# Performance work log

Hardware: AMD Instinct MI355X
Metric: run time of the kernel (lower is better)

The kernel has to match this reference:

```python
import jax, jax.numpy as jnp
import numpy as np

N = 50000          # nodes
E = 1_600_000      # edges (avg degree 32)
IN = 128           # in_channels
H1, C1 = 4, 8      # conv1: heads=4, out=8 -> concat 32
OUT = 64           # out_channels (conv2, heads=1)
NEG_SLOPE = 0.2    # PyG GATConv default LeakyReLU slope


def _gat_layer(x, edge_index, W, att_src, att_dst, bias, heads, out_ch):
    """PyG-style GATConv (concat=True, add_self_loops=True).
    x: [N, F_in], edge_index: [2, E], W: [F_in, heads*out_ch],
    att_src/att_dst: [heads, out_ch], bias: [heads*out_ch].
    """
    n = x.shape[0]
    loops = jnp.arange(n)
    src = jnp.concatenate([edge_index[0], loops])  # message source j
    dst = jnp.concatenate([edge_index[1], loops])  # aggregation target i

    h = (x @ W).reshape(n, heads, out_ch)                 # [N, H, C]
    a_src = jnp.sum(h * att_src, axis=-1)                 # [N, H]
    a_dst = jnp.sum(h * att_dst, axis=-1)                 # [N, H]

    logits = jax.nn.leaky_relu(a_src[src] + a_dst[dst], NEG_SLOPE)  # [E', H]
    # segment softmax over incoming edges of each destination node
    m = jax.ops.segment_max(logits, dst, num_segments=n)            # [N, H]
    e = jnp.exp(logits - m[dst])
    s = jax.ops.segment_sum(e, dst, num_segments=n)                 # [N, H]
    alpha = e / (s[dst] + 1e-16)                                    # [E', H]

    msg = h[src] * alpha[..., None]                                 # [E', H, C]
    out = jax.ops.segment_sum(msg, dst, num_segments=n)             # [N, H, C]
    return out.reshape(n, heads * out_ch) + bias


def setup_inputs() -> dict:
    key = jax.random.key(0)
    ks = jax.random.split(key, 10)
    g = 0.1
    x = jax.random.normal(ks[0], (N, IN), jnp.float32)
    edge_index = jax.random.randint(ks[1], (2, E), 0, N, dtype=jnp.int64)
    W1 = jax.random.normal(ks[2], (IN, H1 * C1), jnp.float32) * g
    att_src1 = jax.random.normal(ks[3], (H1, C1), jnp.float32) * g
    att_dst1 = jax.random.normal(ks[4], (H1, C1), jnp.float32) * g
    b1 = jnp.zeros((H1 * C1,), jnp.float32)
    W2 = jax.random.normal(ks[5], (H1 * C1, OUT), jnp.float32) * g
    att_src2 = jax.random.normal(ks[6], (1, OUT), jnp.float32) * g
    att_dst2 = jax.random.normal(ks[7], (1, OUT), jnp.float32) * g
    b2 = jnp.zeros((OUT,), jnp.float32)
    return {"x": x, "edge_index": edge_index,
            "W1": W1, "att_src1": att_src1, "att_dst1": att_dst1, "b1": b1,
            "W2": W2, "att_src2": att_src2, "att_dst2": att_dst2, "b2": b2}


def reference(x, edge_index, W1, att_src1, att_dst1, b1, W2, att_src2, att_dst2, b2):
    h = _gat_layer(x, edge_index, W1, att_src1, att_dst1, b1, H1, C1)   # [N, 32]
    h = jax.nn.relu(h)
    out = _gat_layer(h, edge_index, W2, att_src2, att_dst2, b2, 1, OUT)  # [N, 64]
    return out
```

## Files before the change

kernel.cpp:

```cpp
#include <hip/hip_runtime.h>
#include <hip/hip_bf16.h>

#define IN_CH 128
#define H1C1  32
#define NH1   4
#define OUTC  64
#define NEG   0.2f
#define RPAD  16
#define BSH   6
#define BSZ   64
#define NBMAX 1024
#define CHUNK 4096
#define CAP   3072
#define PCAP  4096
#define NPB   32

typedef __hip_bfloat16 bf16;
typedef unsigned int u32;
typedef unsigned short u16;

__device__ __forceinline__ u16 f2bf_bits(float f) {
  bf16 v = __float2bfloat16(f);
  return *(u16*)&v;
}
__device__ __forceinline__ float bflo(u32 g) { return __uint_as_float(g << 16); }
__device__ __forceinline__ float bfhi(u32 g) { return __uint_as_float(g & 0xFFFF0000u); }

__global__ __launch_bounds__(256) void k_bin_tr(
    const int* __restrict__ ei, int* __restrict__ bucket_fill,
    u32* __restrict__ data, int E, int n, int nb, int nA,
    const float* __restrict__ x, const float* __restrict__ W1,
    const float* __restrict__ as1, const float* __restrict__ ad1,
    u16* __restrict__ h1b, float* __restrict__ a_src, float* __restrict__ a_dst) {
  __shared__ __align__(16) char smem[28672];
  int t = threadIdx.x;
  if ((int)blockIdx.x < nA) {
    int* cnt   = (int*)smem;
    int* lbase = cnt + NBMAX;
    int* gbase = lbase + NBMAX;
    u32* staged = (u32*)(gbase + NBMAX);
    int lane = t & 63, wid = t >> 6;
    for (int b = t; b < nb; b += 256) cnt[b] = 0;
    __syncthreads();
    long base = (long)blockIdx.x * CHUNK;
    long totE = (long)E + n;
    u32 pk[CHUNK / 256];
    int bk[CHUNK / 256];
#pragma unroll
    for (int i = 0; i < CHUNK / 256; i++) {
      long e = base + i * 256 + t;
      if (e < totE) {
        int j, d;
        if (e < E) {
          j = ei[e]; d = ei[E + e];
          j = j < 0 ? 0 : (j >= n ? n - 1 : j);
          d = d < 0 ? 0 : (d >= n ? n - 1 : d);
        } else { j = d = (int)(e - E); }
        bk[i] = d >> BSH;
        pk[i] = ((u32)d << 16) | (u32)j;
        atomicAdd(&cnt[bk[i]], 1);
      } else bk[i] = -1;
    }
    __syncthreads();
    if (wid == 0) {
      int carry = 0;
      for (int b0 = 0; b0 < nb; b0 += 64) {
        int i = b0 + lane;
        int v = (i < nb) ? cnt[i] : 0;
        int orig = v;
        for (int off = 1; off < 64; off <<= 1) {
          int u = __shfl_up(v, off, 64);
          if (lane >= off) v += u;
        }
        if (i < nb) lbase[i] = carry + v - orig;
        carry += __shfl(v, 63, 64);
      }
    }
    __syncthreads();
    for (int b = t; b < nb; b += 256) {
      int c = cnt[b];
      gbase[b] = c ? atomicAdd(&bucket_fill[b], c) : 0;
      cnt[b] = 0;
    }
    __syncthreads();
#pragma unroll
    for (int i = 0; i < CHUNK / 256; i++) {
      if (bk[i] >= 0) {
        int loc = atomicAdd(&cnt[bk[i]], 1);
        staged[lbase[bk[i]] + loc] = pk[i];
      }
    }
    __syncthreads();
    long remL = totE - base;
    int rem = remL > CHUNK ? CHUNK : (int)remL;
    for (int idx = t; idx < rem; idx += 256) {
      u32 p = staged[idx];
      int b = (int)(p >> 16) >> BSH;
      int off2 = gbase[b] + (idx - lbase[b]);
      if (off2 < CAP) data[(size_t)b * CAP + off2] = p;
    }
  } else {
    float* xs = (float*)smem;
    int base = ((int)blockIdx.x - nA) * NPB;
    for (int i4 = t; i4 < NPB * 32; i4 += 256) {
      int nd = base + (i4 >> 5);
      float4 v = make_float4(0.f, 0.f, 0.f, 0.f);
      if (nd < n) v = ((const float4*)x)[(size_t)base * 32 + i4];
      ((float4*)xs)[i4] = v;
    }
    int mg = t & 7, ks = (t >> 3) & 7, ns = t >> 6;
    int m0 = mg * 4;
    float4 w[4][4];
#pragma unroll
    for (int kk = 0; kk < 4; kk++) {
      int q = (kk + ks) & 3;
      int k0 = ks * 16 + q * 4;
      float4 t0 = *(const float4*)(W1 + (k0 + 0) * H1C1 + m0);
      float4 t1 = *(const float4*)(W1 + (k0 + 1) * H1C1 + m0);
      float4 t2 = *(const float4*)(W1 + (k0 + 2) * H1C1 + m0);
      float4 t3 = *(const float4*)(W1 + (k0 + 3) * H1C1 + m0);
      w[kk][0] = make_float4(t0.x, t1.x, t2.x, t3.x);
      w[kk][1] = make_float4(t0.y, t1.y, t2.y, t3.y);
      w[kk][2] = make_float4(t0.z, t1.z, t2.z, t3.z);
      w[kk][3] = make_float4(t0.w, t1.w, t2.w, t3.w);
    }
    float4 asq = *(const float4*)(as1 + m0);
    float4 adq = *(const float4*)(ad1 + m0);
    __syncthreads();
#pragma unroll 2
    for (int r = 0; r < 8; r++) {
      int nl = r * 4 + ns;
      const float4* xrow = (const float4*)(xs + nl * IN_CH + ks * 16);
      float a0 = 0.f, a1 = 0.f, a2 = 0.f, a3 = 0.f;
#pragma unroll
      for (int kk = 0; kk < 4; kk++) {
        int q = (kk + ks) & 3;
        float4 xv = xrow[q];
        a0 += xv.x * w[kk][0].x + xv.y * w[kk][0].y + xv.z * w[kk][0].z + xv.w * w[kk][0].w;
        a1 += xv.x * w[kk][1].x + xv.y * w[kk][1].y + xv.z * w[kk][1].z + xv.w * w[kk][1].w;
        a2 += xv.x * w[kk][2].x + xv.y * w[kk][2].y + xv.z * w[kk][2].z + xv.w * w[kk][2].w;
        a3 += xv.x * w[kk][3].x + xv.y * w[kk][3].y + xv.z * w[kk][3].z + xv.w * w[kk][3].w;
      }
#pragma unroll
      for (int off = 8; off < 64; off <<= 1) {
        a0 += __shfl_xor(a0, off, 64);
        a1 += __shfl_xor(a1, off, 64);
        a2 += __shfl_xor(a2, off, 64);
        a3 += __shfl_xor(a3, off, 64);
      }
      int node = base + nl;
      if (ks == 0 && node < n) {
        float vs = a0 * asq.x + a1 * asq.y + a2 * asq.z + a3 * asq.w;
        float vd = a0 * adq.x + a1 * adq.y + a2 * adq.z + a3 * adq.w;
        vs += __shfl_xor(vs, 1, 64);
        vd += __shfl_xor(vd, 1, 64);
        u32 lo = (u32)f2bf_bits(a0) | ((u32)f2bf_bits(a1) << 16);
        u32 hi = (u32)f2bf_bits(a2) | ((u32)f2bf_bits(a3) << 16);
        *(uint2*)(h1b + (size_t)node * H1C1 + m0) = make_uint2(lo, hi);
        if ((mg & 1) == 0) {
          a_src[node * NH1 + (mg >> 1)] = vs;
          a_dst[node * NH1 + (mg >> 1)] = vd;
        }
      }
    }
    if ((int)blockIdx.x == nA) {
      if (t < H1C1) h1b[n * H1C1 + t] = 0;
      if (t < NH1)  a_src[n * NH1 + t] = -1e30f;
    }
  }
}

__global__ __launch_bounds__(256) void k_bucket_scatter(
    const u32* __restrict__ data, const int* __restrict__ bucket_fill,
    int2* __restrict__ rowse, int* __restrict__ col, int n) {
  __shared__ int cur[BSZ];
  __shared__ int rp[BSZ];
  __shared__ int pd[BSZ];
  int t = threadIdx.x;
  int b = blockIdx.x;
  if (t < BSZ) cur[t] = 0;
  __syncthreads();
  int s = b * CAP;
  int cnt = bucket_fill[b];
  if (cnt > CAP) cnt = CAP;
  for (int i = t; i < cnt; i += 256)
    atomicAdd(&cur[(data[s + i] >> 16) & (BSZ - 1)], 1);
  __syncthreads();
  if (t < 64) {
    int raw = cur[t];
    int v = (raw + RPAD - 1) & ~(RPAD - 1);
    int orig = v;
    for (int off = 1; off < 64; off <<= 1) {
      int u = __shfl_up(v, off, 64);
      if (t >= off) v += u;
    }
    int r = b * PCAP + v - orig;
    rp[t] = r;
    pd[t] = orig;
    cur[t] = r;
    int node = (b << BSH) + t;
    if (node < n) rowse[node] = make_int2(r, r + orig);
  }
  __syncthreads();
  for (int i = t; i < cnt; i += 256) {
    u32 p = data[s + i];
    int dl = (int)(p >> 16) & (BSZ - 1);
    int pos = atomicAdd(&cur[dl], 1);
    col[pos] = (int)(p & 0xFFFFu);
  }
  __syncthreads();
  if (t < 64) {
    int c = cur[t];
    int end = rp[t] + pd[t];
    for (int k = c; k < end; k++) col[k] = n;
  }
}

__global__ __launch_bounds__(256) void k_l1_agg(
    const int2* __restrict__ rowse, const int* __restrict__ col,
    const u16* __restrict__ h1b, const float* __restrict__ a_src,
    const float* __restrict__ a_dst, const float* __restrict__ b1,
    const float* __restrict__ W2, const float* __restrict__ as2,
    const float* __restrict__ ad2,
    u16* __restrict__ h2, float* __restrict__ a_src2, float* __restrict__ a_dst2,
    int n) {
  __shared__ float W2s[8 * 256];
  __shared__ float hsh[16][H1C1];
  __shared__ int   js[4][64];
  __shared__ float wsh[4][NH1][68];
  int t = threadIdx.x;
  int wid = t >> 6, lane = t & 63;
  {
    int c = t & 63;
#pragma unroll
    for (int g = 0; g < 2; g++) {
      int kg = (t >> 6) + 4 * g;
      float4 v;
      v.x = W2[(kg * 4 + 0) * OUTC + c];
      v.y = W2[(kg * 4 + 1) * OUTC + c];
      v.z = W2[(kg * 4 + 2) * OUTC + c];
      v.w = W2[(kg * 4 + 3) * OUTC + c];
      *(float4*)(W2s + kg * 256 + c * 4) = v;
    }
  }
  int o = lane >> 3, u = lane & 7;
  int hd = u >> 1;
  for (int s = 0; s < 4; s++) {
    int node = blockIdx.x * 16 + wid * 4 + s;
    if (node >= n) continue;
    int2 se = rowse[node];
    int rs = se.x, re = se.y;
    float4 ad = *(const float4*)(a_dst + node * NH1);
    float a0 = 0.f, a1 = 0.f, a2 = 0.f, a3 = 0.f, sw = 0.f;
    for (int tb = rs; tb < re; tb += 64) {
      int kmax = re - tb; if (kmax > 64) kmax = 64;
      if (lane < kmax) {
        int j = col[tb + lane];
        float4 as = *(const float4*)(a_src + j * NH1);
        float l0 = as.x + ad.x; l0 = l0 > 0.f ? l0 : NEG * l0;
        float l1 = as.y + ad.y; l1 = l1 > 0.f ? l1 : NEG * l1;
        float l2 = as.z + ad.z; l2 = l2 > 0.f ? l2 : NEG * l2;
        float l3 = as.w + ad.w; l3 = l3 > 0.f ? l3 : NEG * l3;
        js[wid][lane] = j;
        wsh[wid][0][lane] = __expf(l0);
        wsh[wid][1][lane] = __expf(l1);
        wsh[wid][2][lane] = __expf(l2);
        wsh[wid][3][lane] = __expf(l3);
      }
      int nbod = kmax >> 4;
      uint2 G0[4], G1[4];
      float W0[4], W1v[4];
#pragma unroll
      for (int b = 0; b < 4; b++) {
        if (b < nbod) {
          int k = b * 16;
          int j0 = js[wid][k + o];
          int j1 = js[wid][k + 8 + o];
          W0[b]  = wsh[wid][hd][k + o];
          W1v[b] = wsh[wid][hd][k + 8 + o];
          G0[b] = *(const uint2*)(h1b + j0 * H1C1 + 4 * u);
          G1[b] = *(const uint2*)(h1b + j1 * H1C1 + 4 * u);
        }
      }
#pragma unroll
      for (int b = 0; b < 4; b++) {
        if (b < nbod) {
          float w0 = W0[b], w1 = W1v[b];
          uint2 g0 = G0[b], g1 = G1[b];
          a0 += w0 * bflo(g0.x) + w1 * bflo(g1.x);
          a1 += w0 * bfhi(g0.x) + w1 * bfhi(g1.x);
          a2 += w0 * bflo(g0.y) + w1 * bflo(g1.y);
          a3 += w0 * bfhi(g0.y) + w1 * bfhi(g1.y);
          sw += w0 + w1;
        }
      }
    }
    for (int off = 8; off < 64; off <<= 1) {
      a0 += __shfl_xor(a0, off, 64);
      a1 += __shfl_xor(a1, off, 64);
      a2 += __shfl_xor(a2, off, 64);
      a3 += __shfl_xor(a3, off, 64);
      sw += __shfl_xor(sw, off, 64);
    }
    if (o == 0) {
      float inv = 1.f / (sw + 1e-16f);
      int c = 4 * u;
      hsh[wid * 4 + s][c]     = fmaxf(a0 * inv + b1[c], 0.f);
      hsh[wid * 4 + s][c + 1] = fmaxf(a1 * inv + b1[c + 1], 0.f);
      hsh[wid * 4 + s][c + 2] = fmaxf(a2 * inv + b1[c + 2], 0.f);
      hsh[wid * 4 + s][c + 3] = fmaxf(a3 * inv + b1[c + 3], 0.f);
    }
  }
  __syncthreads();
  float as2l = as2[lane], ad2l = ad2[lane];
  for (int r = 0; r < 4; r++) {
    int nl = wid * 4 + r;
    int node = blockIdx.x * 16 + nl;
    float acc = 0.f;
#pragma unroll
    for (int kg = 0; kg < 8; kg++) {
      float4 hv = *(const float4*)(&hsh[nl][kg * 4]);
      float4 wv = *(const float4*)(W2s + kg * 256 + lane * 4);
      acc += hv.x * wv.x + hv.y * wv.y + hv.z * wv.z + hv.w * wv.w;
    }
    float vs = acc * as2l;
    float vd = acc * ad2l;
    for (int off = 1; off < 64; off <<= 1) {
      vs += __shfl_xor(vs, off, 64);
      vd += __shfl_xor(vd, off, 64);
    }
    if (node < n) {
      h2[node * OUTC + lane] = f2bf_bits(acc);
      if (lane == 0) { a_src2[node] = vs; a_dst2[node] = vd; }
    }
  }
  if (blockIdx.x == 0) {
    if (t < OUTC) h2[n * OUTC + t] = 0;
    if (t == 0)   a_src2[n] = -1e30f;
  }
}

__global__ __launch_bounds__(256) void k_l2_agg(
    const int2* __restrict__ rowse, const int* __restrict__ col,
    const u16* __restrict__ h2, const float* __restrict__ a_src2,
    const float* __restrict__ a_dst2, const float* __restrict__ b2v,
    float* __restrict__ out, int n) {
  __shared__ int   js[4][64];
  __shared__ float wsh[4][64];
  int t = threadIdx.x;
  int wid = t >> 6, lane = t & 63;
  int o = lane >> 4, u = lane & 15;
  for (int s = 0; s < 4; s++) {
    int node = blockIdx.x * 16 + wid * 4 + s;
    if (node >= n) continue;
    int2 se = rowse[node];
    int rs = se.x, re = se.y;
    float ad = a_dst2[node];
    float a0 = 0.f, a1 = 0.f, a2 = 0.f, a3 = 0.f, sw = 0.f;
    for (int tb = rs; tb < re; tb += 64) {
      int kmax = re - tb; if (kmax > 64) kmax = 64;
      if (lane < kmax) {
        int j = col[tb + lane];
        float lg = a_src2[j] + ad;
        lg = lg > 0.f ? lg : NEG * lg;
        js[wid][lane] = j;
        wsh[wid][lane] = __expf(lg);
      }
      int nbod = kmax >> 4;
      for (int kb = 0; kb < nbod; kb += 2) {
        int np = (kb + 1 < nbod) ? 2 : 1;
        uint2 G[2][4];
        float W[2][4];
#pragma unroll
        for (int p = 0; p < 2; p++) {
          if (p < np) {
            int k = (kb + p) * 16;
#pragma unroll
            for (int q = 0; q < 4; q++) {
              int j = js[wid][k + 4 * q + o];
              W[p][q] = wsh[wid][k + 4 * q + o];
              G[p][q] = *(const uint2*)(h2 + j * OUTC + 4 * u);
            }
          }
        }
#pragma unroll
        for (int p = 0; p < 2; p++) {
          if (p < np) {
            a0 += W[p][0] * bflo(G[p][0].x) + W[p][1] * bflo(G[p][1].x);
            a0 += W[p][2] * bflo(G[p][2].x) + W[p][3] * bflo(G[p][3].x);
            a1 += W[p][0] * bfhi(G[p][0].x) + W[p][1] * bfhi(G[p][1].x);
            a1 += W[p][2] * bfhi(G[p][2].x) + W[p][3] * bfhi(G[p][3].x);
            a2 += W[p][0] * bflo(G[p][0].y) + W[p][1] * bflo(G[p][1].y);
            a2 += W[p][2] * bflo(G[p][2].y) + W[p][3] * bflo(G[p][3].y);
            a3 += W[p][0] * bfhi(G[p][0].y) + W[p][1] * bfhi(G[p][1].y);
            a3 += W[p][2] * bfhi(G[p][2].y) + W[p][3] * bfhi(G[p][3].y);
            sw += (W[p][0] + W[p][1]) + (W[p][2] + W[p][3]);
          }
        }
      }
    }
    for (int off = 16; off < 64; off <<= 1) {
      a0 += __shfl_xor(a0, off, 64);
      a1 += __shfl_xor(a1, off, 64);
      a2 += __shfl_xor(a2, off, 64);
      a3 += __shfl_xor(a3, off, 64);
      sw += __shfl_xor(sw, off, 64);
    }
    if (o == 0) {
      float inv = 1.f / (sw + 1e-16f);
      int c = 4 * u;
      float4 ov;
      ov.x = a0 * inv + b2v[c];
      ov.y = a1 * inv + b2v[c + 1];
      ov.z = a2 * inv + b2v[c + 2];
      ov.w = a3 * inv + b2v[c + 3];
      *(float4*)(out + node * OUTC + c) = ov;
    }
  }
}


extern "C" void kernel_launch(void* const* d_in, const int* in_sizes, int n_in,
                              void* d_out, int out_size, void* d_ws, size_t ws_size,
                              hipStream_t stream) {
  const float* x   = (const float*)d_in[0];
  const int*   ei  = (const int*)d_in[1];
  const float* W1  = (const float*)d_in[2];
  const float* as1 = (const float*)d_in[3];
  const float* ad1 = (const float*)d_in[4];
  const float* b1  = (const float*)d_in[5];
  const float* W2  = (const float*)d_in[6];
  const float* as2 = (const float*)d_in[7];
  const float* ad2 = (const float*)d_in[8];
  const float* b2  = (const float*)d_in[9];
  float* out = (float*)d_out;

  int n = in_sizes[0] / IN_CH;
  int E = in_sizes[1] / 2;
  int nb = (n + BSZ - 1) >> BSH;
  long tot = (long)E + n;
  int nA = (int)((tot + CHUNK - 1) / CHUNK);
  int nTr = (n + NPB - 1) / NPB;

  char* w = (char*)d_ws;
  auto al = [](size_t v) { return (v + 255) & ~(size_t)255; };
  size_t off = 0;
  int*  bucket_fill = (int*)(w + off);  off += al((size_t)nb * 4);
  int2* rowse       = (int2*)(w + off); off += al((size_t)(n + 1) * 8);
  u32*  data        = (u32*)(w + off);  off += al((size_t)nb * CAP * 4);
  int*  col         = (int*)(w + off);  off += al((size_t)nb * PCAP * 4);
  u16*  h1b         = (u16*)(w + off);  off += al((size_t)(n + 1) * H1C1 * 2);
  float* a_src1     = (float*)(w + off); off += al((size_t)(n + 1) * NH1 * 4);
  float* a_dst1     = (float*)(w + off); off += al((size_t)(n + 1) * NH1 * 4);
  u16*  h2          = (u16*)(w + off);  off += al((size_t)(n + 1) * OUTC * 2);
  float* a_src2     = (float*)(w + off); off += al((size_t)(n + 1) * 4);
  float* a_dst2     = (float*)(w + off); off += al((size_t)(n + 1) * 4);

  hipMemsetAsync(bucket_fill, 0, (size_t)nb * 4, stream);
  hipLaunchKernelGGL(k_bin_tr, dim3(nA + nTr), dim3(256), 0, stream,
                     ei, bucket_fill, data, E, n, nb, nA,
                     x, W1, as1, ad1, h1b, a_src1, a_dst1);
  hipLaunchKernelGGL(k_bucket_scatter, dim3(nb), dim3(256), 0, stream,
                     data, bucket_fill, rowse, col, n);

  hipLaunchKernelGGL(k_l1_agg, dim3((n + 15) / 16), dim3(256), 0, stream,
                     rowse, col, h1b, a_src1, a_dst1, b1,
                     W2, as2, ad2, h2, a_src2, a_dst2, n);

  hipLaunchKernelGGL(k_l2_agg, dim3((n + 15) / 16), dim3(256), 0, stream,
                     rowse, col, h2, a_src2, a_dst2, b2, out, n);
}
```

Baseline: 206.5 us.

## Batch first-chunk edge prologue across four nodes per wave in GAT aggregation

Both aggregation kernels now load row ranges, the first 64 column indices, and the attention scalars for all four nodes a wave handles before any gather starts. The exp weights go into per-node shared buffers, so the dependent loads of the four nodes overlap instead of being serialized node by node. Indices are stored pre-shifted as byte offsets, which removes address multiplies from the gather loop. The cost is more shared memory and more registers per wave, and rows longer than 64 still fall back to a per-chunk loop.

```diff
diff --git a/kernel.cpp b/kernel.cpp
--- a/kernel.cpp
+++ b/kernel.cpp
@@ -226,8 +226,8 @@
     int n) {
   __shared__ float W2s[8 * 256];
   __shared__ float hsh[16][H1C1];
-  __shared__ int   js[4][64];
-  __shared__ float wsh[4][NH1][68];
+  __shared__ int   js[4][4][64];
+  __shared__ float wsh[4][4][NH1][68];
   int t = threadIdx.x;
   int wid = t >> 6, lane = t & 63;
   {
@@ -245,48 +245,97 @@
   }
   int o = lane >> 3, u = lane & 7;
   int hd = u >> 1;
-  for (int s = 0; s < 4; s++) {
-    int node = blockIdx.x * 16 + wid * 4 + s;
-    if (node >= n) continue;
-    int2 se = rowse[node];
-    int rs = se.x, re = se.y;
-    float4 ad = *(const float4*)(a_dst + node * NH1);
+  const char* h1p = (const char*)h1b + 8 * u;
+  int node0 = blockIdx.x * 16 + wid * 4;
+  int rs[4], re[4], jv[4];
+  float4 adv[4];
+#pragma unroll
+  for (int s = 0; s < 4; s++) {
+    int nd = node0 + s;
+    int2 se = make_int2(0, 0);
+    if (nd < n) se = rowse[nd];
+    rs[s] = se.x; re[s] = se.y;
+  }
+#pragma unroll
+  for (int s = 0; s < 4; s++) {
+    int k1 = re[s] - rs[s]; if (k1 > 64) k1 = 64;
+    jv[s] = (lane < k1) ? col[rs[s] + lane] : n;
+  }
+#pragma unroll
+  for (int s = 0; s < 4; s++) {
+    int nd = node0 + s; int ndc = nd < n ? nd : 0;
+    adv[s] = *(const float4*)(a_dst + ndc * NH1);
+  }
+  float4 asv[4];
+#pragma unroll
+  for (int s = 0; s < 4; s++) asv[s] = *(const float4*)(a_src + jv[s] * NH1);
+#pragma unroll
+  for (int s = 0; s < 4; s++) {
+    float l0 = asv[s].x + adv[s].x; l0 = l0 > 0.f ? l0 : NEG * l0;
+    float l1 = asv[s].y + adv[s].y; l1 = l1 > 0.f ? l1 : NEG * l1;
+    float l2 = asv[s].z + adv[s].z; l2 = l2 > 0.f ? l2 : NEG * l2;
+    float l3 = asv[s].w + adv[s].w; l3 = l3 > 0.f ? l3 : NEG * l3;
+    js[wid][s][lane] = jv[s] << 6;
+    wsh[wid][s][0][lane] = __expf(l0);
+    wsh[wid][s][1][lane] = __expf(l1);
+    wsh[wid][s][2][lane] = __expf(l2);
+    wsh[wid][s][3][lane] = __expf(l3);
+  }
+#pragma unroll
+  for (int s = 0; s < 4; s++) {
     float a0 = 0.f, a1 = 0.f, a2 = 0.f, a3 = 0.f, sw = 0.f;
-    for (int tb = rs; tb < re; tb += 64) {
-      int kmax = re - tb; if (kmax > 64) kmax = 64;
-      if (lane < kmax) {
-        int j = col[tb + lane];
-        float4 as = *(const float4*)(a_src + j * NH1);
-        float l0 = as.x + ad.x; l0 = l0 > 0.f ? l0 : NEG * l0;
-        float l1 = as.y + ad.y; l1 = l1 > 0.f ? l1 : NEG * l1;
-        float l2 = as.z + ad.z; l2 = l2 > 0.f ? l2 : NEG * l2;
-        float l3 = as.w + ad.w; l3 = l3 > 0.f ? l3 : NEG * l3;
-        js[wid][lane] = j;
-        wsh[wid][0][lane] = __expf(l0);
-        wsh[wid][1][lane] = __expf(l1);
-        wsh[wid][2][lane] = __expf(l2);
-        wsh[wid][3][lane] = __expf(l3);
-      }
-      int nbod = kmax >> 4;
-      uint2 G0[4], G1[4];
-      float W0[4], W1v[4];
+    int k1 = re[s] - rs[s]; if (k1 > 64) k1 = 64;
+    int nbod = k1 >> 4;
+    uint2 G0[4], G1[4];
+    float W0[4], W1v[4];
+#pragma unroll
+    for (int b = 0; b < 4; b++) {
+      if (b < nbod) {
+        int k = b * 16;
+        int j0 = js[wid][s][k + o];
+        int j1 = js[wid][s][k + 8 + o];
+        W0[b]  = wsh[wid][s][hd][k + o];
+        W1v[b] = wsh[wid][s][hd][k + 8 + o];
+        G0[b] = *(const uint2*)(h1p + j0);
+        G1[b] = *(const uint2*)(h1p + j1);
+      }
+    }
+#pragma unroll
+    for (int b = 0; b < 4; b++) {
+      if (b < nbod) {
+        float w0 = W0[b], w1 = W1v[b];
+        uint2 g0 = G0[b], g1 = G1[b];
+        a0 += w0 * bflo(g0.x) + w1 * bflo(g1.x);
+        a1 += w0 * bfhi(g0.x) + w1 * bfhi(g1.x);
+        a2 += w0 * bflo(g0.y) + w1 * bflo(g1.y);
+        a3 += w0 * bfhi(g0.y) + w1 * bfhi(g1.y);
+        sw += w0 + w1;
+      }
+    }
+    for (int tb = rs[s] + 64; tb < re[s]; tb += 64) {
+      int kmax = re[s] - tb; if (kmax > 64) kmax = 64;
+      int jx = (lane < kmax) ? col[tb + lane] : n;
+      float4 as = *(const float4*)(a_src + jx * NH1);
+      float l0 = as.x + adv[s].x; l0 = l0 > 0.f ? l0 : NEG * l0;
+      float l1 = as.y + adv[s].y; l1 = l1 > 0.f ? l1 : NEG * l1;
+      float l2 = as.z + adv[s].z; l2 = l2 > 0.f ? l2 : NEG * l2;
+      float l3 = as.w + adv[s].w; l3 = l3 > 0.f ? l3 : NEG * l3;
+      js[wid][s][lane] = jx << 6;
+      wsh[wid][s][0][lane] = __expf(l0);
+      wsh[wid][s][1][lane] = __expf(l1);
+      wsh[wid][s][2][lane] = __expf(l2);
+      wsh[wid][s][3][lane] = __expf(l3);
+      int nb2 = kmax >> 4;
 #pragma unroll
       for (int b = 0; b < 4; b++) {
-        if (b < nbod) {
+        if (b < nb2) {
           int k = b * 16;
-          int j0 = js[wid][k + o];
-          int j1 = js[wid][k + 8 + o];
-          W0[b]  = wsh[wid][hd][k + o];
-          W1v[b] = wsh[wid][hd][k + 8 + o];
-          G0[b] = *(const uint2*)(h1b + j0 * H1C1 + 4 * u);
-          G1[b] = *(const uint2*)(h1b + j1 * H1C1 + 4 * u);
-        }
-      }
-#pragma unroll
-      for (int b = 0; b < 4; b++) {
-        if (b < nbod) {
-          float w0 = W0[b], w1 = W1v[b];
-          uint2 g0 = G0[b], g1 = G1[b];
+          int j0 = js[wid][s][k + o];
+          int j1 = js[wid][s][k + 8 + o];
+          float w0 = wsh[wid][s][hd][k + o];
+          float w1 = wsh[wid][s][hd][k + 8 + o];
+          uint2 g0 = *(const uint2*)(h1p + j0);
+          uint2 g1 = *(const uint2*)(h1p + j1);
           a0 += w0 * bflo(g0.x) + w1 * bflo(g1.x);
           a1 += w0 * bfhi(g0.x) + w1 * bfhi(g1.x);
           a2 += w0 * bflo(g0.y) + w1 * bflo(g1.y);
@@ -345,57 +394,98 @@
     const u16* __restrict__ h2, const float* __restrict__ a_src2,
     const float* __restrict__ a_dst2, const float* __restrict__ b2v,
     float* __restrict__ out, int n) {
-  __shared__ int   js[4][64];
-  __shared__ float wsh[4][64];
+  __shared__ int   js[4][4][64];
+  __shared__ float wsh[4][4][64];
   int t = threadIdx.x;
   int wid = t >> 6, lane = t & 63;
   int o = lane >> 4, u = lane & 15;
-  for (int s = 0; s < 4; s++) {
-    int node = blockIdx.x * 16 + wid * 4 + s;
-    if (node >= n) continue;
-    int2 se = rowse[node];
-    int rs = se.x, re = se.y;
-    float ad = a_dst2[node];
+  const char* h2p = (const char*)h2 + 8 * u;
+  int node0 = blockIdx.x * 16 + wid * 4;
+  int rs[4], re[4], jv[4];
+  float adv[4];
+#pragma unroll
+  for (int s = 0; s < 4; s++) {
+    int nd = node0 + s;
+    int2 se = make_int2(0, 0);
+    if (nd < n) se = rowse[nd];
+    rs[s] = se.x; re[s] = se.y;
+  }
+#pragma unroll
+  for (int s = 0; s < 4; s++) {
+    int k1 = re[s] - rs[s]; if (k1 > 64) k1 = 64;
+    jv[s] = (lane < k1) ? col[rs[s] + lane] : n;
+  }
+#pragma unroll
+  for (int s = 0; s < 4; s++) {
+    int nd = node0 + s; int ndc = nd < n ? nd : 0;
+    adv[s] = a_dst2[ndc];
+  }
+  float asv[4];
+#pragma unroll
+  for (int s = 0; s < 4; s++) asv[s] = a_src2[jv[s]];
+#pragma unroll
+  for (int s = 0; s < 4; s++) {
+    float lg = asv[s] + adv[s];
+    lg = lg > 0.f ? lg : NEG * lg;
+    js[wid][s][lane] = jv[s] << 7;
+    wsh[wid][s][lane] = __expf(lg);
+  }
+#pragma unroll
+  for (int s = 0; s < 4; s++) {
+    int node = node0 + s;
     float a0 = 0.f, a1 = 0.f, a2 = 0.f, a3 = 0.f, sw = 0.f;
-    for (int tb = rs; tb < re; tb += 64) {
-      int kmax = re - tb; if (kmax > 64) kmax = 64;
-      if (lane < kmax) {
-        int j = col[tb + lane];
-        float lg = a_src2[j] + ad;
-        lg = lg > 0.f ? lg : NEG * lg;
-        js[wid][lane] = j;
-        wsh[wid][lane] = __expf(lg);
-      }
-      int nbod = kmax >> 4;
-      for (int kb = 0; kb < nbod; kb += 2) {
-        int np = (kb + 1 < nbod) ? 2 : 1;
-        uint2 G[2][4];
-        float W[2][4];
-#pragma unroll
-        for (int p = 0; p < 2; p++) {
-          if (p < np) {
-            int k = (kb + p) * 16;
-#pragma unroll
-            for (int q = 0; q < 4; q++) {
-              int j = js[wid][k + 4 * q + o];
-              W[p][q] = wsh[wid][k + 4 * q + o];
-              G[p][q] = *(const uint2*)(h2 + j * OUTC + 4 * u);
-            }
-          }
+    int k1 = re[s] - rs[s]; if (k1 > 64) k1 = 64;
+    int nbod = k1 >> 4;
+    uint2 G[4][4];
+    float W[4][4];
+#pragma unroll
+    for (int b = 0; b < 4; b++) {
+      if (b < nbod) {
+#pragma unroll
+        for (int q = 0; q < 4; q++) {
+          int e = b * 16 + 4 * q + o;
+          W[b][q] = wsh[wid][s][e];
+          G[b][q] = *(const uint2*)(h2p + js[wid][s][e]);
         }
-#pragma unroll
-        for (int p = 0; p < 2; p++) {
-          if (p < np) {
-            a0 += W[p][0] * bflo(G[p][0].x) + W[p][1] * bflo(G[p][1].x);
-            a0 += W[p][2] * bflo(G[p][2].x) + W[p][3] * bflo(G[p][3].x);
-            a1 += W[p][0] * bfhi(G[p][0].x) + W[p][1] * bfhi(G[p][1].x);
-            a1 += W[p][2] * bfhi(G[p][2].x) + W[p][3] * bfhi(G[p][3].x);
-            a2 += W[p][0] * bflo(G[p][0].y) + W[p][1] * bflo(G[p][1].y);
-            a2 += W[p][2] * bflo(G[p][2].y) + W[p][3] * bflo(G[p][3].y);
-            a3 += W[p][0] * bfhi(G[p][0].y) + W[p][1] * bfhi(G[p][1].y);
-            a3 += W[p][2] * bfhi(G[p][2].y) + W[p][3] * bfhi(G[p][3].y);
-            sw += (W[p][0] + W[p][1]) + (W[p][2] + W[p][3]);
-          }
+      }
+    }
+#pragma unroll
+    for (int b = 0; b < 4; b++) {
+      if (b < nbod) {
+        a0 += W[b][0] * bflo(G[b][0].x) + W[b][1] * bflo(G[b][1].x);
+        a0 += W[b][2] * bflo(G[b][2].x) + W[b][3] * bflo(G[b][3].x);
+        a1 += W[b][0] * bfhi(G[b][0].x) + W[b][1] * bfhi(G[b][1].x);
+        a1 += W[b][2] * bfhi(G[b][2].x) + W[b][3] * bfhi(G[b][3].x);
+        a2 += W[b][0] * bflo(G[b][0].y) + W[b][1] * bflo(G[b][1].y);
+        a2 += W[b][2] * bflo(G[b][2].y) + W[b][3] * bflo(G[b][3].y);
+        a3 += W[b][0] * bfhi(G[b][0].y) + W[b][1] * bfhi(G[b][1].y);
+        a3 += W[b][2] * bfhi(G[b][2].y) + W[b][3] * bfhi(G[b][3].y);
+        sw += (W[b][0] + W[b][1]) + (W[b][2] + W[b][3]);
+      }
+    }
+    for (int tb = rs[s] + 64; tb < re[s]; tb += 64) {
+      int kmax = re[s] - tb; if (kmax > 64) kmax = 64;
+      int jx = (lane < kmax) ? col[tb + lane] : n;
+      float lg = a_src2[jx] + adv[s];
+      lg = lg > 0.f ? lg : NEG * lg;
+      js[wid][s][lane] = jx << 7;
+      wsh[wid][s][lane] = __expf(lg);
+      int nb2 = kmax >> 4;
+#pragma unroll
+      for (int b = 0; b < 4; b++) {
+        if (b < nb2) {
+          float w0, w1, w2, w3;
+          uint2 g0, g1, g2, g3;
+          int k = b * 16;
+          w0 = wsh[wid][s][k + o];      g0 = *(const uint2*)(h2p + js[wid][s][k + o]);
+          w1 = wsh[wid][s][k + 4 + o];  g1 = *(const uint2*)(h2p + js[wid][s][k + 4 + o]);
+          w2 = wsh[wid][s][k + 8 + o];  g2 = *(const uint2*)(h2p + js[wid][s][k + 8 + o]);
+          w3 = wsh[wid][s][k + 12 + o]; g3 = *(const uint2*)(h2p + js[wid][s][k + 12 + o]);
+          a0 += w0 * bflo(g0.x) + w1 * bflo(g1.x) + w2 * bflo(g2.x) + w3 * bflo(g3.x);
+          a1 += w0 * bfhi(g0.x) + w1 * bfhi(g1.x) + w2 * bfhi(g2.x) + w3 * bfhi(g3.x);
+          a2 += w0 * bflo(g0.y) + w1 * bflo(g1.y) + w2 * bflo(g2.y) + w3 * bflo(g3.y);
+          a3 += w0 * bfhi(g0.y) + w1 * bfhi(g1.y) + w2 * bfhi(g2.y) + w3 * bfhi(g3.y);
+          sw += (w0 + w1) + (w2 + w3);
         }
       }
     }
@@ -406,7 +496,7 @@
       a3 += __shfl_xor(a3, off, 64);
       sw += __shfl_xor(sw, off, 64);
     }
-    if (o == 0) {
+    if (o == 0 && node < n) {
       float inv = 1.f / (sw + 1e-16f);
       int c = 4 * u;
       float4 ov;
```

After: 212.4 us. 1.03x slower.
